# Kernel optimization log

Hardware: AMD Instinct MI355X
Metric: run time of the kernel (lower is better)

Reference implementation:

```python
import jax, jax.numpy as jnp
import numpy as np

NUM_ITEM = 80000
NUM_USER = 20000
N = NUM_ITEM + NUM_USER
E = 1_000_000
DIM_FEAT = 64
USER_DIM = 128
DIM_ID = 64
SLOPE = 0.01  # F.leaky_relu default negative_slope


def setup_inputs() -> dict:
    key = jax.random.key(0)
    ks = jax.random.split(key, 16)
    s = 0.05
    # self-loop-free random edge list (torch code removes self loops)
    src = jax.random.randint(ks[0], (E,), 0, N)
    off = jax.random.randint(ks[1], (E,), 1, N)
    dst = (src + off) % N
    edge_index = jnp.stack([src, dst]).astype(jnp.int32)
    return {
        "features": jax.random.normal(ks[2], (NUM_ITEM, DIM_FEAT), jnp.float32),
        "user_features": jax.random.normal(ks[3], (NUM_USER, USER_DIM), jnp.float32),
        "id_embedding_weight": jax.random.normal(ks[4], (N, DIM_ID), jnp.float32) * s,
        "user_mlp_w": jax.random.normal(ks[5], (DIM_FEAT, USER_DIM), jnp.float32) * s,
        "user_mlp_b": jnp.zeros((DIM_FEAT,), jnp.float32),
        "gat1_w": jax.random.normal(ks[6], (DIM_FEAT, DIM_FEAT), jnp.float32) * s,
        "lin1_w": jax.random.normal(ks[7], (DIM_ID, DIM_FEAT), jnp.float32) * s,
        "lin1_b": jnp.zeros((DIM_ID,), jnp.float32),
        "g1_w": jax.random.normal(ks[8], (DIM_ID, DIM_FEAT), jnp.float32) * s,
        "g1_b": jnp.zeros((DIM_ID,), jnp.float32),
        "gat2_w": jax.random.normal(ks[9], (DIM_ID, DIM_ID), jnp.float32) * s,
        "lin2_w": jax.random.normal(ks[10], (DIM_ID, DIM_ID), jnp.float32) * s,
        "lin2_b": jnp.zeros((DIM_ID,), jnp.float32),
        "g2_w": jax.random.normal(ks[11], (DIM_ID, DIM_ID), jnp.float32) * s,
        "g2_b": jnp.zeros((DIM_ID,), jnp.float32),
        "edge_index": edge_index,
    }


def leaky_relu(x):
    return jnp.where(x >= 0, x, SLOPE * x)


def graph_gat(x, W, src, dst):
    """GraphGAT layer (MGAT-style): x@W, inner-product attention with
    degree-based sigmoid gate, edge softmax over target nodes, scatter-add."""
    n = x.shape[0]
    xw = x @ W                                   # [N, d_out]
    x_i = xw[dst]                                # gathered target feats [E, d]
    x_j = xw[src]                                # gathered source feats [E, d]
    inner = jnp.sum(x_i * x_j, axis=-1)          # [E]
    deg = jnp.zeros((n,), xw.dtype).at[src].add(1.0)
    dinv = deg[src] ** -0.5                      # deg[src] >= 1 by construction
    gate = jax.nn.sigmoid(dinv * inner)
    logits = inner * gate
    # segment softmax over destination index (PyG softmax)
    m = jax.ops.segment_max(logits, dst, num_segments=n)
    m = jnp.where(jnp.isfinite(m), m, 0.0)
    e = jnp.exp(logits - m[dst])
    z = jax.ops.segment_sum(e, dst, num_segments=n)
    attn = e / (z[dst] + 1e-16)
    msg = x_j * attn[:, None]                    # [E, d]
    return jnp.zeros_like(xw).at[dst].add(msg)   # scatter-add aggr


def reference(features, user_features, id_embedding_weight,
              user_mlp_w, user_mlp_b,
              gat1_w, lin1_w, lin1_b, g1_w, g1_b,
              gat2_w, lin2_w, lin2_b, g2_w, g2_b,
              edge_index):
    src, dst = edge_index[0], edge_index[1]
    user = jnp.tanh(user_features @ user_mlp_w.T + user_mlp_b)
    x = jnp.concatenate([features, user], axis=0)          # [N, dim_feat]
    nrm = jnp.linalg.norm(x, axis=-1, keepdims=True)
    x = x / jnp.maximum(nrm, 1e-12)                        # F.normalize

    # hop 1
    h = leaky_relu(graph_gat(x, gat1_w, src, dst))
    x_hat = leaky_relu(x @ lin1_w.T + lin1_b) + id_embedding_weight
    x1 = leaky_relu(h @ g1_w.T + g1_b + x_hat)

    # hop 2
    h = leaky_relu(graph_gat(x1, gat2_w, src, dst))
    x_hat = leaky_relu(x1 @ lin2_w.T + lin2_b) + id_embedding_weight
    x2 = leaky_relu(h @ g2_w.T + g2_b + x_hat)

    return jnp.concatenate([x1, x2], axis=1)               # [N, 2*dim_id]
```

## Files before the change

kernel.cpp:

```cpp
#include <hip/hip_runtime.h>
#include <hip/hip_bf16.h>
#include <hip/hip_fp16.h>

#define N_ITEM 80000
#define N_USER 20000
#define NN     100000
#define NE     1000000
#define SCAN_T 1024
#define SCAN_TILES ((NN + SCAN_T - 1) / SCAN_T)

typedef __hip_bfloat16 bf16;

__device__ __forceinline__ float b2f(bf16 v) { return __bfloat162float(v); }
__device__ __forceinline__ bf16  f2b(float v) { return __float2bfloat16(v); }
__device__ __forceinline__ float bits2f(unsigned short h) {
    return __uint_as_float(((unsigned)h) << 16);
}
__device__ __forceinline__ float leaky(float v) { return v >= 0.f ? v : 0.01f * v; }

template<typename T>
__device__ __forceinline__ float ldT(const void* p, size_t i);
template<> __device__ __forceinline__ float ldT<float>(const void* p, size_t i) {
    return ((const float*)p)[i];
}
template<> __device__ __forceinline__ float ldT<bf16>(const void* p, size_t i) {
    return b2f(((const bf16*)p)[i]);
}
template<typename T>
__device__ __forceinline__ float4 ldT4(const void* p, size_t i);
template<> __device__ __forceinline__ float4 ldT4<float>(const void* p, size_t i) {
    return *(const float4*)((const float*)p + i);
}
template<> __device__ __forceinline__ float4 ldT4<bf16>(const void* p, size_t i) {
    ushort4 u = *(const ushort4*)((const unsigned short*)p + i);
    return make_float4(bits2f(u.x), bits2f(u.y), bits2f(u.z), bits2f(u.w));
}
template<typename T>
__device__ __forceinline__ void stT4(void* p, size_t i, float4 v);
template<> __device__ __forceinline__ void stT4<float>(void* p, size_t i, float4 v) {
    *(float4*)((float*)p + i) = v;
}
template<> __device__ __forceinline__ void stT4<bf16>(void* p, size_t i, float4 v) {
    bf16 b0 = f2b(v.x), b1 = f2b(v.y), b2 = f2b(v.z), b3 = f2b(v.w);
    ushort4 u = make_ushort4(*(unsigned short*)&b0, *(unsigned short*)&b1,
                             *(unsigned short*)&b2, *(unsigned short*)&b3);
    *(ushort4*)((unsigned short*)p + i) = u;
}
__device__ __forceinline__ float4 ld4f(const float* p, size_t i) {
    return *(const float4*)(p + i);
}
__device__ __forceinline__ float4 ld4b(const unsigned short* p, size_t i) {
    ushort4 u = *(const ushort4*)(p + i);
    return make_float4(bits2f(u.x), bits2f(u.y), bits2f(u.z), bits2f(u.w));
}
__device__ __forceinline__ void st4b(unsigned short* p, size_t i, float4 v) {
    bf16 b0 = f2b(v.x), b1 = f2b(v.y), b2 = f2b(v.z), b3 = f2b(v.w);
    ushort4 u = make_ushort4(*(unsigned short*)&b0, *(unsigned short*)&b1,
                             *(unsigned short*)&b2, *(unsigned short*)&b3);
    *(ushort4*)(p + i) = u;
}
__device__ __forceinline__ float4 ld4h(const unsigned short* p, size_t i) {
    ushort4 u = *(const ushort4*)(p + i);
    __half h0, h1, h2, h3;
    *(unsigned short*)&h0 = u.x; *(unsigned short*)&h1 = u.y;
    *(unsigned short*)&h2 = u.z; *(unsigned short*)&h3 = u.w;
    return make_float4(__half2float(h0), __half2float(h1),
                       __half2float(h2), __half2float(h3));
}
__device__ __forceinline__ void st4h(unsigned short* p, size_t i, float4 v) {
    __half h0 = __float2half(v.x), h1 = __float2half(v.y);
    __half h2 = __float2half(v.z), h3 = __float2half(v.w);
    ushort4 u = make_ushort4(*(unsigned short*)&h0, *(unsigned short*)&h1,
                             *(unsigned short*)&h2, *(unsigned short*)&h3);
    *(ushort4*)(p + i) = u;
}

__device__ __forceinline__ float wred(float v) {
    for (int o = 32; o; o >>= 1) v += __shfl_xor(v, o, 64);
    return v;
}
__device__ __forceinline__ float gred16(float v) {
    for (int o = 8; o; o >>= 1) v += __shfl_xor(v, o, 64);
    return v;
}
__device__ __forceinline__ int wscan(int v, int lane) {
    for (int o = 1; o < 64; o <<= 1) {
        int t = __shfl_up(v, o, 64);
        v += (lane >= o) ? t : 0;
    }
    return v;
}

__global__ void k_detect(const unsigned short* __restrict__ w, int* __restrict__ mode) {
    __shared__ int cnt[256];
    int bad = 0;
    for (int i = threadIdx.x; i < 4096; i += 256) {
        unsigned e = (w[i] >> 7) & 0xFFu;
        bad += (e == 0u || e == 0xFFu) ? 1 : 0;
    }
    cnt[threadIdx.x] = bad;
    __syncthreads();
    if (threadIdx.x == 0) {
        int t = 0;
        for (int k = 0; k < 256; k++) t += cnt[k];
        mode[0] = (t > 0) ? 1 : 0;
    }
}

__global__ void k_prep_w(const void* umw, const void* lw1, const void* gw1,
                         const void* lw2, const void* gw2,
                         float* umwT, float* wT, const int* mode) {
    int t = blockIdx.x * 256 + threadIdx.x;
    bool f32m = (*mode != 0);
    if (t < 8192) {
        int j = t >> 7, k = t & 127;
        float v = f32m ? ldT<float>(umw, t) : ldT<bf16>(umw, t);
        umwT[k * 64 + j] = v;
    } else {
        int u = t - 8192;
        int m = u >> 12;
        int r = u & 4095;
        int j = r >> 6, k = r & 63;
        const void* srcp = (m == 0) ? lw1 : (m == 1) ? gw1 : (m == 2) ? lw2 : gw2;
        float v = f32m ? ldT<float>(srcp, r) : ldT<bf16>(srcp, r);
        wT[m * 4096 + k * 64 + j] = v;
    }
}

__global__ void k_deg(const int* __restrict__ src, const int* __restrict__ dst,
                      int* __restrict__ deg, int* __restrict__ cnt) {
    int e = blockIdx.x * blockDim.x + threadIdx.x;
    if (e < NE) {
        atomicAdd(&deg[src[e]], 1);
        atomicAdd(&cnt[dst[e]], 1);
    }
}

__global__ void k_dinv(const int* __restrict__ deg, float* __restrict__ dinv) {
    int i = blockIdx.x * blockDim.x + threadIdx.x;
    if (i < NN) dinv[i] = rsqrtf((float)max(deg[i], 1));
}

__global__ void k_scan_sum(const int* __restrict__ cnt, int* __restrict__ tsum) {
    __shared__ int wsum[16];
    int i = blockIdx.x * SCAN_T + threadIdx.x;
    int lane = threadIdx.x & 63, wid = threadIdx.x >> 6;
    int v = (i < NN) ? cnt[i] : 0;
    float s = wred((float)v);
    if (lane == 0) wsum[wid] = (int)s;
    __syncthreads();
    if (threadIdx.x == 0) {
        int t = 0;
        #pragma unroll
        for (int k = 0; k < 16; k++) t += wsum[k];
        tsum[blockIdx.x] = t;
    }
}

__global__ void k_scan_tiles(const int* __restrict__ tsum, int* __restrict__ toff) {
    __shared__ int wsum[16];
    int lane = threadIdx.x & 63, wid = threadIdx.x >> 6;
    int v = (threadIdx.x < SCAN_TILES) ? tsum[threadIdx.x] : 0;
    int inc = wscan(v, lane);
    if (lane == 63) wsum[wid] = inc;
    __syncthreads();
    if (wid == 0) {
        int ws = (lane < 16) ? wsum[lane] : 0;
        int wi = wscan(ws, lane);
        if (lane < 16) wsum[lane] = wi - ws;
    }
    __syncthreads();
    if (threadIdx.x < SCAN_TILES) toff[threadIdx.x] = inc - v + wsum[wid];
}

__global__ void k_scan_out(const int* __restrict__ cnt, const int* __restrict__ toff,
                           int* __restrict__ csr_off, int* __restrict__ cursor) {
    __shared__ int wsum[16];
    int i = blockIdx.x * SCAN_T + threadIdx.x;
    int lane = threadIdx.x & 63, wid = threadIdx.x >> 6;
    int v = (i < NN) ? cnt[i] : 0;
    int inc = wscan(v, lane);
    if (lane == 63) wsum[wid] = inc;
    __syncthreads();
    if (wid == 0) {
        int ws = (lane < 16) ? wsum[lane] : 0;
        int wi = wscan(ws, lane);
        if (lane < 16) wsum[lane] = wi - ws;
    }
    __syncthreads();
    int excl = inc - v + wsum[wid] + toff[blockIdx.x];
    if (i < NN) { csr_off[i] = excl; cursor[i] = excl; }
    if (i == NN - 1) csr_off[NN] = excl + v;
}

__global__ void k_scatter(const int* __restrict__ src, const int* __restrict__ dst,
                          int* __restrict__ cursor, int* __restrict__ csr_src) {
    int e = blockIdx.x * blockDim.x + threadIdx.x;
    if (e < NE) {
        int pos = atomicAdd(&cursor[dst[e]], 1);
        csr_src[pos] = src[e];
    }
}

template<typename T>
__device__ __forceinline__ void prep_items_body(const void* feat, float* x) {
    int i = blockIdx.x * 4 + (threadIdx.x >> 6);
    int j = threadIdx.x & 63;
    if (i >= N_ITEM) return;
    float v = ldT<T>(feat, (size_t)i * 64 + j);
    float ss = wred(v * v);
    float inv = 1.f / fmaxf(sqrtf(ss), 1e-12f);
    x[(size_t)i * 64 + j] = v * inv;
}
__global__ void k_prep_items(const void* feat, float* x, const int* mode) {
    if (*mode) prep_items_body<float>(feat, x);
    else       prep_items_body<bf16>(feat, x);
}

template<typename T>
__device__ __forceinline__ void prep_users_body(const void* uf, const float* wT,
                                                const void* b, float* x) {
    int u = blockIdx.x * 4 + (threadIdx.x >> 6);
    int j = threadIdx.x & 63;
    if (u >= N_USER) return;
    size_t ub = (size_t)u * 128;
    float acc = ldT<T>(b, j);
    #pragma unroll 8
    for (int k = 0; k < 128; k++)
        acc += ldT<T>(uf, ub + k) * wT[k * 64 + j];
    float v = tanhf(acc);
    float ss = wred(v * v);
    float inv = 1.f / fmaxf(sqrtf(ss), 1e-12f);
    x[(size_t)(N_ITEM + u) * 64 + j] = v * inv;
}
__global__ void k_prep_users(const void* uf, const float* wT, const void* b,
                             float* x, const int* mode) {
    if (*mode) prep_users_body<float>(uf, wT, b, x);
    else       prep_users_body<bf16>(uf, wT, b, x);
}

template<typename T>
__device__ __forceinline__ void pre_body(const float* __restrict__ xin,
                                         const void* __restrict__ Wg,
                                         const float* __restrict__ lT,
                                         const void* __restrict__ lb,
                                         const void* __restrict__ id_emb,
                                         unsigned short* __restrict__ xw,
                                         unsigned short* __restrict__ xhat) {
    __shared__ float4 gsW[1024];
    __shared__ float4 gsL[1024];
    int lane = threadIdx.x & 63, wid = threadIdx.x >> 6;
    int sl = lane & 15;
    int i = blockIdx.x * 16 + (wid << 2) + (lane >> 4);
    #pragma unroll
    for (int t = 0; t < 4; t++) {
        int idx = threadIdx.x + t * 256;
        gsW[idx] = ldT4<T>(Wg, (size_t)idx * 4);
        gsL[idx] = ld4f(lT, (size_t)idx * 4);
    }
    size_t rb = (size_t)i * 64 + sl * 4;
    float4 xv = ld4f(xin, rb);
    float4 lb4 = ldT4<T>(lb, sl * 4);
    float4 id4 = ldT4<T>(id_emb, rb);
    __syncthreads();
    float4 accw = make_float4(0.f, 0.f, 0.f, 0.f);
    float4 accl = make_float4(0.f, 0.f, 0.f, 0.f);
    int gbase = lane & 48;
    #pragma unroll
    for (int kk = 0; kk < 16; kk++) {
        int srcl = gbase | kk;
        float xb[4];
        xb[0] = __shfl(xv.x, srcl, 64);
        xb[1] = __shfl(xv.y, srcl, 64);
        xb[2] = __shfl(xv.z, srcl, 64);
        xb[3] = __shfl(xv.w, srcl, 64);
        #pragma unroll
        for (int q = 0; q < 4; q++) {
            int wb = (kk * 4 + q) * 16 + sl;
            float4 w4 = gsW[wb];
            float4 l4 = gsL[wb];
            accw.x += xb[q] * w4.x; accw.y += xb[q] * w4.y;
            accw.z += xb[q] * w4.z; accw.w += xb[q] * w4.w;
            accl.x += xb[q] * l4.x; accl.y += xb[q] * l4.y;
            accl.z += xb[q] * l4.z; accl.w += xb[q] * l4.w;
        }
    }
    st4b(xw, rb, accw);
    float4 xh;
    xh.x = leaky(accl.x + lb4.x) + id4.x;
    xh.y = leaky(accl.y + lb4.y) + id4.y;
    xh.z = leaky(accl.z + lb4.z) + id4.z;
    xh.w = leaky(accl.w + lb4.w) + id4.w;
    st4h(xhat, rb, xh);
}
__global__ void k_pre(const float* xin, const void* Wg, const float* lT,
                      const void* lb, const void* id_emb,
                      unsigned short* xw, unsigned short* xhat, const int* mode) {
    if (*mode) pre_body<float>(xin, Wg, lT, lb, id_emb, xw, xhat);
    else       pre_body<bf16>(xin, Wg, lT, lb, id_emb, xw, xhat);
}

template<typename T>
__device__ __forceinline__ void gat_body(const unsigned short* __restrict__ xw,
                                         const unsigned short* __restrict__ xhat,
                                         const int* __restrict__ csr_off,
                                         const int* __restrict__ csr_src,
                                         const float* __restrict__ dinv,
                                         const float* __restrict__ gTg,
                                         const void* gb,
                                         float* __restrict__ xnext, void* out,
                                         int off_out) {
    __shared__ float4 gs[1024];
    int lane = threadIdx.x & 63, wid = threadIdx.x >> 6;
    int sl = lane & 15;
    int i = blockIdx.x * 16 + (wid << 2) + (lane >> 4);
    size_t rb = (size_t)i * 64 + sl * 4;
    #pragma unroll
    for (int t = 0; t < 4; t++)
        gs[threadIdx.x + t * 256] = ((const float4*)gTg)[threadIdx.x + t * 256];

    float4 xd = ld4b(xw, rb);
    int e0 = csr_off[i], e1 = csr_off[i + 1];
    int cnt = e1 - e0;
    float m = -1e30f, l = 0.f;
    float4 acc = make_float4(0.f, 0.f, 0.f, 0.f);
    float4 xsA = make_float4(0.f, 0.f, 0.f, 0.f), xsB = xsA;
    float dA = 1.f, dB = 1.f;
    if (cnt > 0) {
        int s0 = csr_src[e0];
        xsA = ld4b(xw, (size_t)s0 * 64 + sl * 4);
        dA = dinv[s0];
    }
    if (cnt > 1) {
        int s1 = csr_src[e0 + 1];
        xsB = ld4b(xw, (size_t)s1 * 64 + sl * 4);
        dB = dinv[s1];
    }
    for (int t = 0; t < cnt; ++t) {
        float4 xs = xsA; float dv = dA;
        xsA = xsB; dA = dB;
        if (t + 2 < cnt) {
            int sn = csr_src[e0 + t + 2];
            xsB = ld4b(xw, (size_t)sn * 64 + sl * 4);
            dB = dinv[sn];
        }
        float p = xd.x * xs.x + xd.y * xs.y + xd.z * xs.z + xd.w * xs.w;
        float inner = gred16(p);
        float gate = 1.f / (1.f + __expf(-dv * inner));
        float logit = inner * gate;
        float mn = fmaxf(m, logit);
        float sc = __expf(m - mn);
        float w  = __expf(logit - mn);
        acc.x = acc.x * sc + w * xs.x;
        acc.y = acc.y * sc + w * xs.y;
        acc.z = acc.z * sc + w * xs.z;
        acc.w = acc.w * sc + w * xs.w;
        l = l * sc + w;
        m = mn;
    }
    float linv = 1.f / (l + 1e-16f);
    float4 hv = make_float4(leaky(acc.x * linv), leaky(acc.y * linv),
                            leaky(acc.z * linv), leaky(acc.w * linv));
    __syncthreads();
    float4 accg = make_float4(0.f, 0.f, 0.f, 0.f);
    int gbase = lane & 48;
    #pragma unroll
    for (int kk = 0; kk < 16; kk++) {
        int srcl = gbase | kk;
        float hb[4];
        hb[0] = __shfl(hv.x, srcl, 64);
        hb[1] = __shfl(hv.y, srcl, 64);
        hb[2] = __shfl(hv.z, srcl, 64);
        hb[3] = __shfl(hv.w, srcl, 64);
        #pragma unroll
        for (int q = 0; q < 4; q++) {
            float4 g4 = gs[(kk * 4 + q) * 16 + sl];
            accg.x += hb[q] * g4.x; accg.y += hb[q] * g4.y;
            accg.z += hb[q] * g4.z; accg.w += hb[q] * g4.w;
        }
    }
    float4 gb4 = ldT4<T>(gb, sl * 4);
    float4 xh4 = ld4h(xhat, rb);
    float4 xn;
    xn.x = leaky(accg.x + gb4.x + xh4.x);
    xn.y = leaky(accg.y + gb4.y + xh4.y);
    xn.z = leaky(accg.z + gb4.z + xh4.z);
    xn.w = leaky(accg.w + gb4.w + xh4.w);
    if (xnext) *(float4*)(xnext + rb) = xn;
    stT4<T>(out, (size_t)i * 128 + off_out + sl * 4, xn);
}
__global__ void k_gat(const unsigned short* xw, const unsigned short* xhat,
                      const int* csr_off, const int* csr_src, const float* dinv,
                      const float* gTg, const void* gb,
                      float* xnext, void* out, int off_out, const int* mode) {
    if (*mode) gat_body<float>(xw, xhat, csr_off, csr_src, dinv, gTg, gb,
                               xnext, out, off_out);
    else       gat_body<bf16>(xw, xhat, csr_off, csr_src, dinv, gTg, gb,
                              xnext, out, off_out);
}

extern "C" void kernel_launch(void* const* d_in, const int* in_sizes, int n_in,
                              void* d_out, int out_size, void* d_ws, size_t ws_size,
                              hipStream_t stream) {
    const void* feat   = d_in[0];
    const void* uf     = d_in[1];
    const void* id_emb = d_in[2];
    const void* umw    = d_in[3];
    const void* umb    = d_in[4];
    const void* gat1   = d_in[5];
    const void* lin1b  = d_in[7];
    const void* g1b    = d_in[9];
    const void* gat2   = d_in[10];
    const void* lin2b  = d_in[12];
    const void* g2b    = d_in[14];
    const int*  ei     = (const int*)d_in[15];
    const int* src = ei;
    const int* dst = ei + NE;

    int*      mode   = (int*)d_ws;
    int*      deg    = (int*)((char*)d_ws + 16);
    int*      cnt    = deg + NN;
    int*      cursor = cnt + NN;
    int*      csr_off = cursor + NN;
    int*      tsum   = csr_off + NN + 16;
    int*      toff   = tsum + 128;
    float*    dinv   = (float*)(toff + 128);
    float*    umwT   = dinv + NN;
    float*    wT     = umwT + 8192;
    int*      csr_src = (int*)(wT + 4 * 4096);
    float*    buf0   = (float*)(csr_src + NE);
    float*    buf2   = buf0 + (size_t)NN * 64;
    unsigned short* xwb   = (unsigned short*)(buf2 + (size_t)NN * 64);
    unsigned short* xhath = xwb + (size_t)NN * 64;

    k_detect<<<1, 256, 0, stream>>>((const unsigned short*)feat, mode);
    k_prep_w<<<96, 256, 0, stream>>>(umw, d_in[6], d_in[8], d_in[11], d_in[13],
                                     umwT, wT, mode);
    hipMemsetAsync(deg, 0, 2 * NN * 4, stream);
    k_deg<<<(NE + 255) / 256, 256, 0, stream>>>(src, dst, deg, cnt);
    k_dinv<<<(NN + 255) / 256, 256, 0, stream>>>(deg, dinv);
    k_scan_sum<<<SCAN_TILES, SCAN_T, 0, stream>>>(cnt, tsum);
    k_scan_tiles<<<1, SCAN_T, 0, stream>>>(tsum, toff);
    k_scan_out<<<SCAN_TILES, SCAN_T, 0, stream>>>(cnt, toff, csr_off, cursor);
    k_scatter<<<(NE + 255) / 256, 256, 0, stream>>>(src, dst, cursor, csr_src);
    k_prep_items<<<(N_ITEM + 3) / 4, 256, 0, stream>>>(feat, buf0, mode);
    k_prep_users<<<(N_USER + 3) / 4, 256, 0, stream>>>(uf, umwT, umb, buf0, mode);

    const float* lT1 = wT;
    const float* gT1 = wT + 4096;
    const float* lT2 = wT + 8192;
    const float* gT2 = wT + 12288;

    int nb = NN / 16;

    k_pre<<<nb, 256, 0, stream>>>(buf0, gat1, lT1, lin1b, id_emb,
                                  xwb, xhath, mode);
    k_gat<<<nb, 256, 0, stream>>>(xwb, xhath, csr_off, csr_src, dinv,
                                  gT1, g1b, buf2, d_out, 0, mode);
    k_pre<<<nb, 256, 0, stream>>>(buf2, gat2, lT2, lin2b, id_emb,
                                  xwb, xhath, mode);
    k_gat<<<nb, 256, 0, stream>>>(xwb, xhath, csr_off, csr_src, dinv,
                                  gT2, g2b, nullptr, d_out, 64, mode);
}
```

Baseline: 681.8 us.

## Fuse input normalization and user MLP into first-hop projection kernel

```diff
diff --git a/kernel.cpp b/kernel.cpp
--- a/kernel.cpp
+++ b/kernel.cpp
@@ -136,16 +136,13 @@
     }
 }
 
-__global__ void k_dinv(const int* __restrict__ deg, float* __restrict__ dinv) {
-    int i = blockIdx.x * blockDim.x + threadIdx.x;
-    if (i < NN) dinv[i] = rsqrtf((float)max(deg[i], 1));
-}
-
-__global__ void k_scan_sum(const int* __restrict__ cnt, int* __restrict__ tsum) {
+__global__ void k_scan_sum(const int* __restrict__ cnt, const int* __restrict__ deg,
+                           float* __restrict__ dinv, int* __restrict__ tsum) {
     __shared__ int wsum[16];
     int i = blockIdx.x * SCAN_T + threadIdx.x;
     int lane = threadIdx.x & 63, wid = threadIdx.x >> 6;
     int v = (i < NN) ? cnt[i] : 0;
+    if (i < NN) dinv[i] = rsqrtf((float)max(deg[i], 1));
     float s = wred((float)v);
     if (lane == 0) wsum[wid] = (int)s;
     __syncthreads();
@@ -203,40 +200,107 @@
 }
 
 template<typename T>
-__device__ __forceinline__ void prep_items_body(const void* feat, float* x) {
-    int i = blockIdx.x * 4 + (threadIdx.x >> 6);
-    int j = threadIdx.x & 63;
-    if (i >= N_ITEM) return;
-    float v = ldT<T>(feat, (size_t)i * 64 + j);
-    float ss = wred(v * v);
-    float inv = 1.f / fmaxf(sqrtf(ss), 1e-12f);
-    x[(size_t)i * 64 + j] = v * inv;
-}
-__global__ void k_prep_items(const void* feat, float* x, const int* mode) {
-    if (*mode) prep_items_body<float>(feat, x);
-    else       prep_items_body<bf16>(feat, x);
-}
-
-template<typename T>
-__device__ __forceinline__ void prep_users_body(const void* uf, const float* wT,
-                                                const void* b, float* x) {
-    int u = blockIdx.x * 4 + (threadIdx.x >> 6);
-    int j = threadIdx.x & 63;
-    if (u >= N_USER) return;
-    size_t ub = (size_t)u * 128;
-    float acc = ldT<T>(b, j);
-    #pragma unroll 8
-    for (int k = 0; k < 128; k++)
-        acc += ldT<T>(uf, ub + k) * wT[k * 64 + j];
-    float v = tanhf(acc);
-    float ss = wred(v * v);
-    float inv = 1.f / fmaxf(sqrtf(ss), 1e-12f);
-    x[(size_t)(N_ITEM + u) * 64 + j] = v * inv;
-}
-__global__ void k_prep_users(const void* uf, const float* wT, const void* b,
-                             float* x, const int* mode) {
-    if (*mode) prep_users_body<float>(uf, wT, b, x);
-    else       prep_users_body<bf16>(uf, wT, b, x);
+__device__ __forceinline__ void front_body(const void* __restrict__ feat,
+                                           const void* __restrict__ uf,
+                                           const float* __restrict__ umwT,
+                                           const void* __restrict__ umb,
+                                           const void* __restrict__ id_emb,
+                                           const void* __restrict__ Wg,
+                                           const float* __restrict__ lT,
+                                           const void* __restrict__ lb,
+                                           unsigned short* __restrict__ xw,
+                                           unsigned short* __restrict__ xhat) {
+    __shared__ float4 gsW[1024];
+    __shared__ float4 gsL[1024];
+    int lane = threadIdx.x & 63, wid = threadIdx.x >> 6;
+    int sl = lane & 15;
+    int i = blockIdx.x * 16 + (wid << 2) + (lane >> 4);
+    int gbase = lane & 48;
+    size_t rb = (size_t)i * 64 + sl * 4;
+    float4 xv;
+    if (blockIdx.x < (N_ITEM / 16)) {
+        float4 v = ldT4<T>(feat, rb);
+        float ss = gred16(v.x * v.x + v.y * v.y + v.z * v.z + v.w * v.w);
+        float inv = 1.f / fmaxf(sqrtf(ss), 1e-12f);
+        xv = make_float4(v.x * inv, v.y * inv, v.z * inv, v.w * inv);
+    } else {
+        #pragma unroll
+        for (int t = 0; t < 4; t++) {
+            int idx = threadIdx.x + t * 256;
+            gsW[idx] = ld4f(umwT, (size_t)idx * 4);
+            gsL[idx] = ld4f(umwT, (size_t)(idx + 1024) * 4);
+        }
+        __syncthreads();
+        int u = i - N_ITEM;
+        size_t ub = (size_t)u * 128;
+        float4 ufa = ldT4<T>(uf, ub + sl * 8);
+        float4 ufb_ = ldT4<T>(uf, ub + sl * 8 + 4);
+        float ufv[8] = { ufa.x, ufa.y, ufa.z, ufa.w,
+                         ufb_.x, ufb_.y, ufb_.z, ufb_.w };
+        float4 acc = ldT4<T>(umb, sl * 4);
+        #pragma unroll
+        for (int kk = 0; kk < 16; kk++) {
+            int srcl = gbase | kk;
+            #pragma unroll
+            for (int r = 0; r < 8; r++) {
+                int k = kk * 8 + r;
+                float ufk = __shfl(ufv[r], srcl, 64);
+                float4 w4 = (k < 64) ? gsW[k * 16 + sl] : gsL[(k - 64) * 16 + sl];
+                acc.x += ufk * w4.x; acc.y += ufk * w4.y;
+                acc.z += ufk * w4.z; acc.w += ufk * w4.w;
+            }
+        }
+        float4 v = make_float4(tanhf(acc.x), tanhf(acc.y),
+                               tanhf(acc.z), tanhf(acc.w));
+        float ss = gred16(v.x * v.x + v.y * v.y + v.z * v.z + v.w * v.w);
+        float inv = 1.f / fmaxf(sqrtf(ss), 1e-12f);
+        xv = make_float4(v.x * inv, v.y * inv, v.z * inv, v.w * inv);
+        __syncthreads();
+    }
+    #pragma unroll
+    for (int t = 0; t < 4; t++) {
+        int idx = threadIdx.x + t * 256;
+        gsW[idx] = ldT4<T>(Wg, (size_t)idx * 4);
+        gsL[idx] = ld4f(lT, (size_t)idx * 4);
+    }
+    float4 lb4 = ldT4<T>(lb, sl * 4);
+    float4 id4 = ldT4<T>(id_emb, rb);
+    __syncthreads();
+    float4 accw = make_float4(0.f, 0.f, 0.f, 0.f);
+    float4 accl = make_float4(0.f, 0.f, 0.f, 0.f);
+    #pragma unroll
+    for (int kk = 0; kk < 16; kk++) {
+        int srcl = gbase | kk;
+        float xb[4];
+        xb[0] = __shfl(xv.x, srcl, 64);
+        xb[1] = __shfl(xv.y, srcl, 64);
+        xb[2] = __shfl(xv.z, srcl, 64);
+        xb[3] = __shfl(xv.w, srcl, 64);
+        #pragma unroll
+        for (int q = 0; q < 4; q++) {
+            int wb = (kk * 4 + q) * 16 + sl;
+            float4 w4 = gsW[wb];
+            float4 l4 = gsL[wb];
+            accw.x += xb[q] * w4.x; accw.y += xb[q] * w4.y;
+            accw.z += xb[q] * w4.z; accw.w += xb[q] * w4.w;
+            accl.x += xb[q] * l4.x; accl.y += xb[q] * l4.y;
+            accl.z += xb[q] * l4.z; accl.w += xb[q] * l4.w;
+        }
+    }
+    st4b(xw, rb, accw);
+    float4 xh;
+    xh.x = leaky(accl.x + lb4.x) + id4.x;
+    xh.y = leaky(accl.y + lb4.y) + id4.y;
+    xh.z = leaky(accl.z + lb4.z) + id4.z;
+    xh.w = leaky(accl.w + lb4.w) + id4.w;
+    st4h(xhat, rb, xh);
+}
+__global__ void k_front(const void* feat, const void* uf, const float* umwT,
+                        const void* umb, const void* id_emb,
+                        const void* Wg, const float* lT, const void* lb,
+                        unsigned short* xw, unsigned short* xhat, const int* mode) {
+    if (*mode) front_body<float>(feat, uf, umwT, umb, id_emb, Wg, lT, lb, xw, xhat);
+    else       front_body<bf16>(feat, uf, umwT, umb, id_emb, Wg, lT, lb, xw, xhat);
 }
 
 template<typename T>
@@ -438,13 +502,10 @@
                                      umwT, wT, mode);
     hipMemsetAsync(deg, 0, 2 * NN * 4, stream);
     k_deg<<<(NE + 255) / 256, 256, 0, stream>>>(src, dst, deg, cnt);
-    k_dinv<<<(NN + 255) / 256, 256, 0, stream>>>(deg, dinv);
-    k_scan_sum<<<SCAN_TILES, SCAN_T, 0, stream>>>(cnt, tsum);
+    k_scan_sum<<<SCAN_TILES, SCAN_T, 0, stream>>>(cnt, deg, dinv, tsum);
     k_scan_tiles<<<1, SCAN_T, 0, stream>>>(tsum, toff);
     k_scan_out<<<SCAN_TILES, SCAN_T, 0, stream>>>(cnt, toff, csr_off, cursor);
     k_scatter<<<(NE + 255) / 256, 256, 0, stream>>>(src, dst, cursor, csr_src);
-    k_prep_items<<<(N_ITEM + 3) / 4, 256, 0, stream>>>(feat, buf0, mode);
-    k_prep_users<<<(N_USER + 3) / 4, 256, 0, stream>>>(uf, umwT, umb, buf0, mode);
 
     const float* lT1 = wT;
     const float* gT1 = wT + 4096;
@@ -453,8 +514,8 @@
 
     int nb = NN / 16;
 
-    k_pre<<<nb, 256, 0, stream>>>(buf0, gat1, lT1, lin1b, id_emb,
-                                  xwb, xhath, mode);
+    k_front<<<nb, 256, 0, stream>>>(feat, uf, umwT, umb, id_emb,
+                                    gat1, lT1, lin1b, xwb, xhath, mode);
     k_gat<<<nb, 256, 0, stream>>>(xwb, xhath, csr_off, csr_src, dinv,
                                   gT1, g1b, buf2, d_out, 0, mode);
     k_pre<<<nb, 256, 0, stream>>>(buf2, gat2, lT2, lin2b, id_emb,
```

Measured after the change: 1.317 ms. 1.93x slower.
